# Kernel optimization log

Hardware: AMD Instinct MI355X
Metric: run time of the kernel (lower is better)

## Reference

```python
import jax, jax.numpy as jnp
import numpy as np

N_HEADS = 16
NEG_BIAS = -1000000000.0


def setup_inputs() -> dict:
    key = jax.random.key(0)
    k1, k2, k3, k4 = jax.random.split(key, 4)
    B, S, D = 2, 2048, 1024
    queries = jax.random.normal(k1, (B, S, D), dtype=jnp.float32)
    keys = jax.random.normal(k2, (B, S, D), dtype=jnp.float32)
    values = jax.random.normal(k3, (B, S, D), dtype=jnp.float32)
    mask = jax.random.randint(k4, (B, S, S), 0, 2, dtype=jnp.int32)
    return {"queries": queries, "keys": keys, "values": values, "mask": mask}


def _split_heads(x):
    B, S, D = x.shape
    return x.reshape(B, S, N_HEADS, D // N_HEADS).transpose(0, 2, 1, 3)  # [B,H,S,d]


def reference(queries, keys, values, mask):
    q = _split_heads(queries)   # [B,H,Sq,d]
    k = _split_heads(keys)      # [B,H,Sk,d]
    v = _split_heads(values)    # [B,H,Sk,d]
    d_head = q.shape[-1]
    # scaled dot product similarity
    sim = jnp.einsum('bhqd,bhkd->bhqk', q, k) / jnp.sqrt(jnp.float32(d_head))
    # additive mask (softmax attention function -> non-hadamard)
    bias = NEG_BIAS * (1.0 - mask.astype(sim.dtype))[:, None]  # [B,1,Sq,Sk]
    sim = sim + bias
    # softmax with max-subtraction (numerically stable, as in original)
    weights = jax.nn.softmax(sim, axis=-1)
    out = jnp.einsum('bhqk,bhkd->bhqd', weights, v)  # [B,H,Sq,d]
    B, H, Sq, d = out.shape
    return out.transpose(0, 2, 1, 3).reshape(B, Sq, H * d)
```

## Files before the change

kernel.cpp:

```cpp
#include <hip/hip_runtime.h>

#define S_LEN 2048
#define D_MODEL 1024
#define DH 64
#define BQ 128
#define BK 128
#define ZSCALE 0.18033688f

using short8 = __attribute__((ext_vector_type(8))) short;
using s4v    = __attribute__((ext_vector_type(4))) short;
using f32x4  = __attribute__((ext_vector_type(4))) float;
using u32x4  = __attribute__((ext_vector_type(4))) unsigned int;

#define BMM(a, b, c) __builtin_amdgcn_mfma_f32_16x16x32_bf16((a), (b), (c), 0, 0, 0)

__device__ __forceinline__ unsigned short f2bf(float x) {
    union { float f; unsigned int u; } c; c.f = x;
    unsigned int u = c.u;
    u += 0x7fffu + ((u >> 16) & 1u);
    return (unsigned short)(u >> 16);
}

__global__ __launch_bounds__(256) void cvt_fused(const float* __restrict__ V,
                                                 const int* __restrict__ M,
                                                 const float* __restrict__ K,
                                                 unsigned short* __restrict__ VT,
                                                 unsigned long long* __restrict__ Mb,
                                                 unsigned short* __restrict__ KB) {
    const int blk = blockIdx.x;
    const int tid = threadIdx.x;
    if (blk < 1024) {
        __shared__ float tsF[64][65];
        const int b  = blk >> 9;
        const int h  = (blk >> 5) & 15;
        const int s0 = (blk & 31) * 64;
        #pragma unroll
        for (int it = 0; it < 2; ++it) {
            int seg = tid + it * 256;
            int s = seg >> 3, d8 = (seg & 7) << 3;
            const float* p = V + (size_t)(b * S_LEN + s0 + s) * D_MODEL + h * DH + d8;
            f32x4 a = *(const f32x4*)p;
            f32x4 c = *(const f32x4*)(p + 4);
            #pragma unroll
            for (int j = 0; j < 4; ++j) { tsF[s][d8 + j] = a[j]; tsF[s][d8 + 4 + j] = c[j]; }
        }
        __syncthreads();
        #pragma unroll
        for (int it = 0; it < 2; ++it) {
            int seg = tid + it * 256;
            int d = seg >> 3, s8 = (seg & 7) << 3;
            short8 w;
            #pragma unroll
            for (int j = 0; j < 8; ++j) w[j] = (short)f2bf(tsF[s8 + j][d]);
            *(short8*)(VT + ((size_t)((b * 16 + h) * 64 + d)) * S_LEN + s0 + s8) = w;
        }
    } else if (blk < 2048) {
        const int pb   = blk - 1024;
        const int wave = tid >> 6, lane = tid & 63;
        const int row  = pb * 4 + wave;
        const int* mp  = M + (size_t)row * S_LEN;
        #pragma unroll 4
        for (int it = 0; it < 32; ++it) {
            int m = mp[it * 64 + lane];
            unsigned long long bal = __ballot(m != 0);
            if (lane == 0) Mb[(size_t)row * 32 + it] = bal;
        }
    } else {
        size_t base = (size_t)(blk - 2048) * 4096;
        #pragma unroll
        for (int it = 0; it < 4; ++it) {
            size_t i = base + ((size_t)(it * 256 + tid)) * 4;
            f32x4 a = *(const f32x4*)(K + i);
            s4v w;
            #pragma unroll
            for (int j = 0; j < 4; ++j) w[j] = (short)f2bf(a[j]);
            *(s4v*)(KB + i) = w;
        }
    }
}

__global__ __launch_bounds__(256) void mha_fwd_v18(
    const float* __restrict__ Q,
    const float* __restrict__ K,
    const unsigned short* __restrict__ KB,
    const unsigned short* __restrict__ VT,
    const unsigned long long* __restrict__ Mb,
    float* __restrict__ O,
    float* __restrict__ PO,
    float* __restrict__ PL,
    int kbf, int split_mode)
{
    __shared__ alignas(16) unsigned short Ks[BK][64];
    __shared__ alignas(16) unsigned short Vt[DH][128];

    const int blk0 = blockIdx.x;
    int blk, b, h, qt, split;
    if (split_mode) {
        blk = ((blk0 & 7) << 7) | (blk0 >> 3);
        b = blk >> 9; h = (blk >> 5) & 15; qt = (blk >> 1) & 15; split = blk & 1;
    } else {
        blk = ((blk0 & 7) << 6) | (blk0 >> 3);
        b = blk >> 8; h = (blk >> 4) & 15; qt = blk & 15; split = 0;
    }
    const int qbase = qt * BQ;
    const int bh  = b * 16 + h;
    const int kb0 = split * (S_LEN / 2);
    const int kbend = split_mode ? kb0 + S_LEN / 2 : S_LEN;

    const int tid  = threadIdx.x;
    const int wave = tid >> 6;
    const int lane = tid & 63;
    const int n16  = lane & 15;
    const int quad = lane >> 4;
    const int bq   = quad << 3;
    const int n7   = n16 & 7;

    const int srow = tid >> 3;
    const int prow = (((srow >> 2) & 1) << 4) | (((srow >> 3) & 3) << 2) | (srow & 3);
    const int vrow = tid >> 4;

    const int kwcol = (((tid & 7) ^ (prow & 7)) << 3);
    const int vwcol = (((tid & 15) ^ vrow) << 3);
    const int krc0  = ((quad ^ n7) << 3);
    const int krc1  = krc0 ^ 32;
    int vrc[4];
    #pragma unroll
    for (int kc = 0; kc < 4; ++kc) vrc[kc] = (((kc * 4 + quad) ^ n16) << 3);

    short8 qf[2][2];
    #pragma unroll
    for (int qg = 0; qg < 2; ++qg) {
        const size_t qoff = (size_t)(b * S_LEN + qbase + wave * 32 + qg * 16 + n16) * D_MODEL
                          + h * DH + quad * 8;
        f32x4 a0 = *(const f32x4*)(Q + qoff);
        f32x4 a1 = *(const f32x4*)(Q + qoff + 4);
        f32x4 a2 = *(const f32x4*)(Q + qoff + 32);
        f32x4 a3 = *(const f32x4*)(Q + qoff + 36);
        short8 q0, q1;
        #pragma unroll
        for (int j = 0; j < 4; ++j) {
            q0[j] = (short)f2bf(a0[j] * ZSCALE); q0[4 + j] = (short)f2bf(a1[j] * ZSCALE);
            q1[j] = (short)f2bf(a2[j] * ZSCALE); q1[4 + j] = (short)f2bf(a3[j] * ZSCALE);
        }
        qf[qg][0] = q0; qf[qg][1] = q1;
    }

    const short8 ones = {0x3F80,0x3F80,0x3F80,0x3F80,0x3F80,0x3F80,0x3F80,0x3F80};

    f32x4 o[2][4], o4[2];
    #pragma unroll
    for (int qg = 0; qg < 2; ++qg) {
        #pragma unroll
        for (int dg = 0; dg < 4; ++dg) o[qg][dg] = f32x4{0.f,0.f,0.f,0.f};
        o4[qg] = f32x4{0.f,0.f,0.f,0.f};
    }

    const unsigned long long* mrow[2];
    #pragma unroll
    for (int qg = 0; qg < 2; ++qg)
        mrow[qg] = Mb + (size_t)(b * S_LEN + qbase + wave * 32 + qg * 16 + n16) * 32;

    const size_t kbase = (size_t)(b * S_LEN) * D_MODEL + h * DH;
    const size_t vbase = (size_t)(bh * 64) * S_LEN;

    short8 ka[4], va[4];
    unsigned long long mw[2][2];
    if (kbf) {
        #pragma unroll
        for (int i = 0; i < 4; ++i)
            ka[i] = *(const short8*)(KB + kbase + (size_t)(kb0 + i * 32 + srow) * D_MODEL + ((tid & 7) << 3));
    } else {
        #pragma unroll
        for (int i = 0; i < 4; ++i) {
            const float* kp = K + kbase + (size_t)(kb0 + i * 32 + srow) * D_MODEL + ((tid & 7) << 3);
            f32x4 p0 = *(const f32x4*)kp, p1 = *(const f32x4*)(kp + 4);
            short8 w;
            #pragma unroll
            for (int j = 0; j < 4; ++j) { w[j] = (short)f2bf(p0[j]); w[4 + j] = (short)f2bf(p1[j]); }
            ka[i] = w;
        }
    }
    #pragma unroll
    for (int i = 0; i < 4; ++i)
        va[i] = *(const short8*)(VT + vbase + (size_t)(vrow + 16 * i) * S_LEN + kb0 + ((tid & 15) << 3));
    {
        const int wi = kb0 >> 6;
        #pragma unroll
        for (int qg = 0; qg < 2; ++qg) { mw[qg][0] = mrow[qg][wi]; mw[qg][1] = mrow[qg][wi + 1]; }
    }

    for (int kb = kb0; kb < kbend; kb += BK) {
        __builtin_amdgcn_s_barrier();
        __builtin_amdgcn_sched_barrier(0);

        #pragma unroll
        for (int i = 0; i < 4; ++i) {
            *(short8*)&Ks[prow + 32 * i][kwcol] = ka[i];
            *(short8*)&Vt[vrow + 16 * i][vwcol] = va[i];
        }

        const int kn = kb + BK;
        const bool more = kn < kbend;
        short8 nka[4], nva[4];
        unsigned long long nmw[2][2];
        if (more) {
            if (kbf) {
                #pragma unroll
                for (int i = 0; i < 4; ++i)
                    nka[i] = *(const short8*)(KB + kbase + (size_t)(kn + i * 32 + srow) * D_MODEL + ((tid & 7) << 3));
            } else {
                #pragma unroll
                for (int i = 0; i < 4; ++i) {
                    const float* kp = K + kbase + (size_t)(kn + i * 32 + srow) * D_MODEL + ((tid & 7) << 3);
                    f32x4 p0 = *(const f32x4*)kp, p1 = *(const f32x4*)(kp + 4);
                    short8 w;
                    #pragma unroll
                    for (int j = 0; j < 4; ++j) { w[j] = (short)f2bf(p0[j]); w[4 + j] = (short)f2bf(p1[j]); }
                    nka[i] = w;
                }
            }
            #pragma unroll
            for (int i = 0; i < 4; ++i)
                nva[i] = *(const short8*)(VT + vbase + (size_t)(vrow + 16 * i) * S_LEN + kn + ((tid & 15) << 3));
            const int wi = kn >> 6;
            #pragma unroll
            for (int qg = 0; qg < 2; ++qg) { nmw[qg][0] = mrow[qg][wi]; nmw[qg][1] = mrow[qg][wi + 1]; }
        }

        unsigned int am[2][4];
        #pragma unroll
        for (int qg = 0; qg < 2; ++qg) {
            am[qg][0] = ((unsigned int)mw[qg][0]) >> bq;
            am[qg][1] = ((unsigned int)(mw[qg][0] >> 32)) >> bq;
            am[qg][2] = ((unsigned int)mw[qg][1]) >> bq;
            am[qg][3] = ((unsigned int)(mw[qg][1] >> 32)) >> bq;
        }

        asm volatile("s_waitcnt lgkmcnt(0)" ::: "memory");
        __builtin_amdgcn_s_barrier();
        __builtin_amdgcn_sched_barrier(0);

        u32x4 Af[2][4];
        auto QKCT = [&](int ct) {
            short8 kf0 = *(const short8*)&Ks[ct * 16 + n16][krc0];
            short8 kf1 = *(const short8*)&Ks[ct * 16 + n16][krc1];
            f32x4 sA = {0.f,0.f,0.f,0.f}, sB = sA;
            sA = BMM(kf0, qf[0][0], sA); sA = BMM(kf1, qf[0][1], sA);
            sB = BMM(kf0, qf[1][0], sB); sB = BMM(kf1, qf[1][1], sB);
            unsigned int puA[4], puB[4];
            #pragma unroll
            for (int r = 0; r < 4; ++r) {
                puA[r] = __float_as_uint(__builtin_amdgcn_exp2f(sA[r]));
                puB[r] = __float_as_uint(__builtin_amdgcn_exp2f(sB[r]));
            }
            const int sel = ct >> 1, sb = (ct & 1) * 4, kc = ct >> 1, ub = (ct & 1) * 2;
            unsigned int nibA = (am[0][sel] >> sb) & 0xFu;
            unsigned int nibB = (am[1][sel] >> sb) & 0xFu;
            unsigned int m8A = ((nibA * 0x00204081u) & 0x01010101u) * 0xFFu;
            unsigned int m8B = ((nibB * 0x00204081u) & 0x01010101u) * 0xFFu;
            Af[0][kc][ub + 0] = __builtin_amdgcn_perm(puA[1], puA[0], 0x07060302u)
                              & __builtin_amdgcn_perm(0u, m8A, 0x01010000u);
            Af[0][kc][ub + 1] = __builtin_amdgcn_perm(puA[3], puA[2], 0x07060302u)
                              & __builtin_amdgcn_perm(0u, m8A, 0x03030202u);
            Af[1][kc][ub + 0] = __builtin_amdgcn_perm(puB[1], puB[0], 0x07060302u)
                              & __builtin_amdgcn_perm(0u, m8B, 0x01010000u);
            Af[1][kc][ub + 1] = __builtin_amdgcn_perm(puB[3], puB[2], 0x07060302u)
                              & __builtin_amdgcn_perm(0u, m8B, 0x03030202u);
        };
        auto PVKC = [&](int kc) {
            short8 v0 = *(const short8*)&Vt[      n16][vrc[kc]];
            short8 v1 = *(const short8*)&Vt[16 + n16][vrc[kc]];
            short8 v2 = *(const short8*)&Vt[32 + n16][vrc[kc]];
            short8 v3 = *(const short8*)&Vt[48 + n16][vrc[kc]];
            union { u32x4 u; short8 s; } c0, c1;
            c0.u = Af[0][kc]; c1.u = Af[1][kc];
            o[0][0] = BMM(c0.s, v0, o[0][0]); o[0][1] = BMM(c0.s, v1, o[0][1]);
            o[0][2] = BMM(c0.s, v2, o[0][2]); o[0][3] = BMM(c0.s, v3, o[0][3]);
            o4[0]   = BMM(c0.s, ones, o4[0]);
            o[1][0] = BMM(c1.s, v0, o[1][0]); o[1][1] = BMM(c1.s, v1, o[1][1]);
            o[1][2] = BMM(c1.s, v2, o[1][2]); o[1][3] = BMM(c1.s, v3, o[1][3]);
            o4[1]   = BMM(c1.s, ones, o4[1]);
        };

        __builtin_amdgcn_s_setprio(1);
        QKCT(0); QKCT(1);
        PVKC(0);
        QKCT(2); QKCT(3);
        PVKC(1);
        QKCT(4); QKCT(5);
        PVKC(2);
        QKCT(6); QKCT(7);
        PVKC(3);
        __builtin_amdgcn_s_setprio(0);

        if (more) {
            #pragma unroll
            for (int i = 0; i < 4; ++i) { ka[i] = nka[i]; va[i] = nva[i]; }
            #pragma unroll
            for (int qg = 0; qg < 2; ++qg) { mw[qg][0] = nmw[qg][0]; mw[qg][1] = nmw[qg][1]; }
        }
    }

    if (PO) {
        const int pblk = (bh * 16 + qt) * 2 + split;
        float* pp = PO + (size_t)pblk * (BQ * DH);
        float* pl = PL + (size_t)pblk * BQ;
        #pragma unroll
        for (int qg = 0; qg < 2; ++qg) {
            #pragma unroll
            for (int r = 0; r < 4; ++r) {
                const int rowin = wave * 32 + qg * 16 + quad * 4 + r;
                float* op = pp + rowin * DH + n16;
                op[0]  = o[qg][0][r];
                op[16] = o[qg][1][r];
                op[32] = o[qg][2][r];
                op[48] = o[qg][3][r];
                if (n16 == 0) pl[rowin] = o4[qg][r];
            }
        }
    } else {
        #pragma unroll
        for (int qg = 0; qg < 2; ++qg) {
            #pragma unroll
            for (int r = 0; r < 4; ++r) {
                float rl = 1.f / o4[qg][r];
                size_t row = (size_t)(b * S_LEN + qbase + wave * 32 + qg * 16 + quad * 4 + r);
                float* op = O + row * D_MODEL + h * DH + n16;
                op[0]  = o[qg][0][r] * rl;
                op[16] = o[qg][1][r] * rl;
                op[32] = o[qg][2][r] * rl;
                op[48] = o[qg][3][r] * rl;
            }
        }
    }
}

__global__ __launch_bounds__(256) void combine_split(
    const float* __restrict__ PO, const float* __restrict__ PL,
    float* __restrict__ O)
{
    const int tq = blockIdx.x;
    const int b = tq >> 8, h = (tq >> 4) & 15, qt = tq & 15;
    const float* p0 = PO + (size_t)tq * 2 * (BQ * DH);
    const float* p1 = p0 + BQ * DH;
    const float* l0 = PL + (size_t)tq * 2 * BQ;
    const float* l1 = l0 + BQ;
    const int t = threadIdx.x;
    #pragma unroll
    for (int k = 0; k < 8; ++k) {
        const int e   = (t + k * 256) * 4;
        const int row = e >> 6, col = e & 63;
        f32x4 a = *(const f32x4*)(p0 + e);
        f32x4 c = *(const f32x4*)(p1 + e);
        const float rl = 1.f / (l0[row] + l1[row]);
        f32x4 r;
        #pragma unroll
        for (int j = 0; j < 4; ++j) r[j] = (a[j] + c[j]) * rl;
        *(f32x4*)(O + (size_t)(b * S_LEN + qt * BQ + row) * D_MODEL + h * DH + col) = r;
    }
}

extern "C" void kernel_launch(void* const* d_in, const int* in_sizes, int n_in,
                              void* d_out, int out_size, void* d_ws, size_t ws_size,
                              hipStream_t stream) {
    const float* Q = (const float*)d_in[0];
    const float* K = (const float*)d_in[1];
    const float* V = (const float*)d_in[2];
    const int*   M = (const int*)d_in[3];
    float*       O = (float*)d_out;

    const size_t NEL = (size_t)2 * S_LEN * D_MODEL;
    const size_t VT_BYTES = NEL * sizeof(unsigned short);
    const size_t KB_BYTES = NEL * sizeof(unsigned short);
    const size_t MB_BYTES = (size_t)2 * S_LEN * 32 * 8;
    const size_t PO_BYTES = (size_t)512 * 2 * BQ * DH * 4;
    const size_t PL_BYTES = (size_t)512 * 2 * BQ * 4;

    if (ws_size >= VT_BYTES + KB_BYTES + MB_BYTES + PO_BYTES + PL_BYTES) {
        unsigned short* VT = (unsigned short*)d_ws;
        unsigned short* KB = (unsigned short*)((char*)d_ws + VT_BYTES);
        unsigned long long* Mb = (unsigned long long*)((char*)d_ws + VT_BYTES + KB_BYTES);
        float* PO = (float*)((char*)d_ws + VT_BYTES + KB_BYTES + MB_BYTES);
        float* PL = (float*)((char*)d_ws + VT_BYTES + KB_BYTES + MB_BYTES + PO_BYTES);
        hipLaunchKernelGGL(cvt_fused, dim3(3072), dim3(256), 0, stream, V, M, K, VT, Mb, KB);
        hipLaunchKernelGGL(mha_fwd_v18, dim3(1024), dim3(256), 0, stream,
                           Q, K, KB, VT, Mb, O, PO, PL, 1, 1);
        hipLaunchKernelGGL(combine_split, dim3(512), dim3(256), 0, stream, PO, PL, O);
    } else if (ws_size >= VT_BYTES + KB_BYTES + MB_BYTES) {
        unsigned short* VT = (unsigned short*)d_ws;
        unsigned short* KB = (unsigned short*)((char*)d_ws + VT_BYTES);
        unsigned long long* Mb = (unsigned long long*)((char*)d_ws + VT_BYTES + KB_BYTES);
        hipLaunchKernelGGL(cvt_fused, dim3(3072), dim3(256), 0, stream, V, M, K, VT, Mb, KB);
        hipLaunchKernelGGL(mha_fwd_v18, dim3(512), dim3(256), 0, stream,
                           Q, K, KB, VT, Mb, O, (float*)0, (float*)0, 1, 0);
    } else {
        unsigned short* VT = (unsigned short*)d_ws;
        unsigned long long* Mb = (unsigned long long*)((char*)d_ws + VT_BYTES);
        hipLaunchKernelGGL(cvt_fused, dim3(2048), dim3(256), 0, stream, V, M, K, VT, Mb, (unsigned short*)0);
        hipLaunchKernelGGL(mha_fwd_v18, dim3(512), dim3(256), 0, stream,
                           Q, K, (const unsigned short*)0, VT, Mb, O, (float*)0, (float*)0, 0, 0);
    }
}
```

Before: 181.4 us.

## Enlarge split-K attention blocks to 512 threads covering 256 query rows

New measurement: 180.7 us. No clear change (-0.4%).

```diff
diff --git a/kernel.cpp b/kernel.cpp
--- a/kernel.cpp
+++ b/kernel.cpp
@@ -3,7 +3,6 @@
 #define S_LEN 2048
 #define D_MODEL 1024
 #define DH 64
-#define BQ 128
 #define BK 128
 #define ZSCALE 0.18033688f
 
@@ -79,33 +78,28 @@
     }
 }
 
-__global__ __launch_bounds__(256) void mha_fwd_v18(
+__global__ __launch_bounds__(512) void mha_fwd_v19(
     const float* __restrict__ Q,
-    const float* __restrict__ K,
     const unsigned short* __restrict__ KB,
     const unsigned short* __restrict__ VT,
     const unsigned long long* __restrict__ Mb,
-    float* __restrict__ O,
     float* __restrict__ PO,
-    float* __restrict__ PL,
-    int kbf, int split_mode)
+    float* __restrict__ PL)
 {
     __shared__ alignas(16) unsigned short Ks[BK][64];
     __shared__ alignas(16) unsigned short Vt[DH][128];
 
     const int blk0 = blockIdx.x;
-    int blk, b, h, qt, split;
-    if (split_mode) {
-        blk = ((blk0 & 7) << 7) | (blk0 >> 3);
-        b = blk >> 9; h = (blk >> 5) & 15; qt = (blk >> 1) & 15; split = blk & 1;
-    } else {
-        blk = ((blk0 & 7) << 6) | (blk0 >> 3);
-        b = blk >> 8; h = (blk >> 4) & 15; qt = blk & 15; split = 0;
-    }
-    const int qbase = qt * BQ;
-    const int bh  = b * 16 + h;
-    const int kb0 = split * (S_LEN / 2);
-    const int kbend = split_mode ? kb0 + S_LEN / 2 : S_LEN;
+    const int blk  = ((blk0 & 7) << 6) | (blk0 >> 3);
+
+    const int b     = blk >> 8;
+    const int h     = (blk >> 4) & 15;
+    const int qt    = (blk >> 1) & 7;
+    const int split = blk & 1;
+    const int qbase = qt * 256;
+    const int bh    = b * 16 + h;
+    const int kb0   = split * (S_LEN / 2);
+    const int kbend = kb0 + S_LEN / 2;
 
     const int tid  = threadIdx.x;
     const int wave = tid >> 6;
@@ -116,11 +110,12 @@
     const int n7   = n16 & 7;
 
     const int srow = tid >> 3;
-    const int prow = (((srow >> 2) & 1) << 4) | (((srow >> 3) & 3) << 2) | (srow & 3);
+    const int prow = ((srow >> 5) << 5) | (((srow >> 2) & 1) << 4)
+                   | (((srow >> 3) & 3) << 2) | (srow & 3);
     const int vrow = tid >> 4;
 
     const int kwcol = (((tid & 7) ^ (prow & 7)) << 3);
-    const int vwcol = (((tid & 15) ^ vrow) << 3);
+    const int vwcol = (((tid & 15) ^ (vrow & 15)) << 3);
     const int krc0  = ((quad ^ n7) << 3);
     const int krc1  = krc0 ^ 32;
     int vrc[4];
@@ -163,26 +158,14 @@
     const size_t kbase = (size_t)(b * S_LEN) * D_MODEL + h * DH;
     const size_t vbase = (size_t)(bh * 64) * S_LEN;
 
-    short8 ka[4], va[4];
+    short8 ka[2], va[2];
     unsigned long long mw[2][2];
-    if (kbf) {
-        #pragma unroll
-        for (int i = 0; i < 4; ++i)
-            ka[i] = *(const short8*)(KB + kbase + (size_t)(kb0 + i * 32 + srow) * D_MODEL + ((tid & 7) << 3));
-    } else {
-        #pragma unroll
-        for (int i = 0; i < 4; ++i) {
-            const float* kp = K + kbase + (size_t)(kb0 + i * 32 + srow) * D_MODEL + ((tid & 7) << 3);
-            f32x4 p0 = *(const f32x4*)kp, p1 = *(const f32x4*)(kp + 4);
-            short8 w;
-            #pragma unroll
-            for (int j = 0; j < 4; ++j) { w[j] = (short)f2bf(p0[j]); w[4 + j] = (short)f2bf(p1[j]); }
-            ka[i] = w;
-        }
-    }
-    #pragma unroll
-    for (int i = 0; i < 4; ++i)
-        va[i] = *(const short8*)(VT + vbase + (size_t)(vrow + 16 * i) * S_LEN + kb0 + ((tid & 15) << 3));
+    #pragma unroll
+    for (int i = 0; i < 2; ++i)
+        ka[i] = *(const short8*)(KB + kbase + (size_t)(kb0 + i * 64 + srow) * D_MODEL + ((tid & 7) << 3));
+    #pragma unroll
+    for (int i = 0; i < 2; ++i)
+        va[i] = *(const short8*)(VT + vbase + (size_t)(vrow + 32 * i) * S_LEN + kb0 + ((tid & 15) << 3));
     {
         const int wi = kb0 >> 6;
         #pragma unroll
@@ -194,34 +177,22 @@
         __builtin_amdgcn_sched_barrier(0);
 
         #pragma unroll
-        for (int i = 0; i < 4; ++i) {
-            *(short8*)&Ks[prow + 32 * i][kwcol] = ka[i];
-            *(short8*)&Vt[vrow + 16 * i][vwcol] = va[i];
+        for (int i = 0; i < 2; ++i) {
+            *(short8*)&Ks[prow + 64 * i][kwcol] = ka[i];
+            *(short8*)&Vt[vrow + 32 * i][vwcol] = va[i];
         }
 
         const int kn = kb + BK;
         const bool more = kn < kbend;
-        short8 nka[4], nva[4];
+        short8 nka[2], nva[2];
         unsigned long long nmw[2][2];
         if (more) {
-            if (kbf) {
-                #pragma unroll
-                for (int i = 0; i < 4; ++i)
-                    nka[i] = *(const short8*)(KB + kbase + (size_t)(kn + i * 32 + srow) * D_MODEL + ((tid & 7) << 3));
-            } else {
-                #pragma unroll
-                for (int i = 0; i < 4; ++i) {
-                    const float* kp = K + kbase + (size_t)(kn + i * 32 + srow) * D_MODEL + ((tid & 7) << 3);
-                    f32x4 p0 = *(const f32x4*)kp, p1 = *(const f32x4*)(kp + 4);
-                    short8 w;
-                    #pragma unroll
-                    for (int j = 0; j < 4; ++j) { w[j] = (short)f2bf(p0[j]); w[4 + j] = (short)f2bf(p1[j]); }
-                    nka[i] = w;
-                }
-            }
-            #pragma unroll
-            for (int i = 0; i < 4; ++i)
-                nva[i] = *(const short8*)(VT + vbase + (size_t)(vrow + 16 * i) * S_LEN + kn + ((tid & 15) << 3));
+            #pragma unroll
+            for (int i = 0; i < 2; ++i)
+                nka[i] = *(const short8*)(KB + kbase + (size_t)(kn + i * 64 + srow) * D_MODEL + ((tid & 7) << 3));
+            #pragma unroll
+            for (int i = 0; i < 2; ++i)
+                nva[i] = *(const short8*)(VT + vbase + (size_t)(vrow + 32 * i) * S_LEN + kn + ((tid & 15) << 3));
             const int wi = kn >> 6;
             #pragma unroll
             for (int qg = 0; qg < 2; ++qg) { nmw[qg][0] = mrow[qg][wi]; nmw[qg][1] = mrow[qg][wi + 1]; }
@@ -295,16 +266,16 @@
 
         if (more) {
             #pragma unroll
-            for (int i = 0; i < 4; ++i) { ka[i] = nka[i]; va[i] = nva[i]; }
+            for (int i = 0; i < 2; ++i) { ka[i] = nka[i]; va[i] = nva[i]; }
             #pragma unroll
             for (int qg = 0; qg < 2; ++qg) { mw[qg][0] = nmw[qg][0]; mw[qg][1] = nmw[qg][1]; }
         }
     }
 
-    if (PO) {
-        const int pblk = (bh * 16 + qt) * 2 + split;
-        float* pp = PO + (size_t)pblk * (BQ * DH);
-        float* pl = PL + (size_t)pblk * BQ;
+    {
+        const int pblk = ((bh * 8 + qt) << 1) + split;
+        float* pp = PO + (size_t)pblk * (256 * DH);
+        float* pl = PL + (size_t)pblk * 256;
         #pragma unroll
         for (int qg = 0; qg < 2; ++qg) {
             #pragma unroll
@@ -318,36 +289,22 @@
                 if (n16 == 0) pl[rowin] = o4[qg][r];
             }
         }
-    } else {
-        #pragma unroll
-        for (int qg = 0; qg < 2; ++qg) {
-            #pragma unroll
-            for (int r = 0; r < 4; ++r) {
-                float rl = 1.f / o4[qg][r];
-                size_t row = (size_t)(b * S_LEN + qbase + wave * 32 + qg * 16 + quad * 4 + r);
-                float* op = O + row * D_MODEL + h * DH + n16;
-                op[0]  = o[qg][0][r] * rl;
-                op[16] = o[qg][1][r] * rl;
-                op[32] = o[qg][2][r] * rl;
-                op[48] = o[qg][3][r] * rl;
-            }
-        }
     }
 }
 
-__global__ __launch_bounds__(256) void combine_split(
+__global__ __launch_bounds__(256) void combine_split2(
     const float* __restrict__ PO, const float* __restrict__ PL,
     float* __restrict__ O)
 {
     const int tq = blockIdx.x;
-    const int b = tq >> 8, h = (tq >> 4) & 15, qt = tq & 15;
-    const float* p0 = PO + (size_t)tq * 2 * (BQ * DH);
-    const float* p1 = p0 + BQ * DH;
-    const float* l0 = PL + (size_t)tq * 2 * BQ;
-    const float* l1 = l0 + BQ;
+    const int b = tq >> 7, h = (tq >> 3) & 15, qt = tq & 7;
+    const float* p0 = PO + (size_t)tq * 2 * (256 * DH);
+    const float* p1 = p0 + 256 * DH;
+    const float* l0 = PL + (size_t)tq * 2 * 256;
+    const float* l1 = l0 + 256;
     const int t = threadIdx.x;
     #pragma unroll
-    for (int k = 0; k < 8; ++k) {
+    for (int k = 0; k < 16; ++k) {
         const int e   = (t + k * 256) * 4;
         const int row = e >> 6, col = e & 63;
         f32x4 a = *(const f32x4*)(p0 + e);
@@ -356,7 +313,227 @@
         f32x4 r;
         #pragma unroll
         for (int j = 0; j < 4; ++j) r[j] = (a[j] + c[j]) * rl;
-        *(f32x4*)(O + (size_t)(b * S_LEN + qt * BQ + row) * D_MODEL + h * DH + col) = r;
+        *(f32x4*)(O + (size_t)(b * S_LEN + qt * 256 + row) * D_MODEL + h * DH + col) = r;
+    }
+}
+
+__global__ __launch_bounds__(256) void mha_fwd_v15f(
+    const float* __restrict__ Q,
+    const float* __restrict__ K,
+    const unsigned short* __restrict__ KB,
+    const unsigned short* __restrict__ VT,
+    const unsigned long long* __restrict__ Mb,
+    float* __restrict__ O,
+    int kbf)
+{
+    __shared__ alignas(16) unsigned short Ks[BK][64];
+    __shared__ alignas(16) unsigned short Vt[DH][128];
+
+    const int blk0 = blockIdx.x;
+    const int blk  = ((blk0 & 7) << 6) | (blk0 >> 3);
+    const int b   = blk >> 8;
+    const int h   = (blk >> 4) & 15;
+    const int qbase = (blk & 15) * 128;
+    const int bh  = b * 16 + h;
+
+    const int tid  = threadIdx.x;
+    const int wave = tid >> 6;
+    const int lane = tid & 63;
+    const int n16  = lane & 15;
+    const int quad = lane >> 4;
+    const int bq   = quad << 3;
+    const int n7   = n16 & 7;
+
+    const int srow = tid >> 3;
+    const int prow = (((srow >> 2) & 1) << 4) | (((srow >> 3) & 3) << 2) | (srow & 3);
+    const int vrow = tid >> 4;
+    const int kwcol = (((tid & 7) ^ (prow & 7)) << 3);
+    const int vwcol = (((tid & 15) ^ vrow) << 3);
+    const int krc0  = ((quad ^ n7) << 3);
+    const int krc1  = krc0 ^ 32;
+    int vrc[4];
+    #pragma unroll
+    for (int kc = 0; kc < 4; ++kc) vrc[kc] = (((kc * 4 + quad) ^ n16) << 3);
+
+    short8 qf[2][2];
+    #pragma unroll
+    for (int qg = 0; qg < 2; ++qg) {
+        const size_t qoff = (size_t)(b * S_LEN + qbase + wave * 32 + qg * 16 + n16) * D_MODEL
+                          + h * DH + quad * 8;
+        f32x4 a0 = *(const f32x4*)(Q + qoff);
+        f32x4 a1 = *(const f32x4*)(Q + qoff + 4);
+        f32x4 a2 = *(const f32x4*)(Q + qoff + 32);
+        f32x4 a3 = *(const f32x4*)(Q + qoff + 36);
+        short8 q0, q1;
+        #pragma unroll
+        for (int j = 0; j < 4; ++j) {
+            q0[j] = (short)f2bf(a0[j] * ZSCALE); q0[4 + j] = (short)f2bf(a1[j] * ZSCALE);
+            q1[j] = (short)f2bf(a2[j] * ZSCALE); q1[4 + j] = (short)f2bf(a3[j] * ZSCALE);
+        }
+        qf[qg][0] = q0; qf[qg][1] = q1;
+    }
+
+    const short8 ones = {0x3F80,0x3F80,0x3F80,0x3F80,0x3F80,0x3F80,0x3F80,0x3F80};
+
+    f32x4 o[2][4], o4[2];
+    #pragma unroll
+    for (int qg = 0; qg < 2; ++qg) {
+        #pragma unroll
+        for (int dg = 0; dg < 4; ++dg) o[qg][dg] = f32x4{0.f,0.f,0.f,0.f};
+        o4[qg] = f32x4{0.f,0.f,0.f,0.f};
+    }
+
+    const unsigned long long* mrow[2];
+    #pragma unroll
+    for (int qg = 0; qg < 2; ++qg)
+        mrow[qg] = Mb + (size_t)(b * S_LEN + qbase + wave * 32 + qg * 16 + n16) * 32;
+
+    const size_t kbase = (size_t)(b * S_LEN) * D_MODEL + h * DH;
+    const size_t vbase = (size_t)(bh * 64) * S_LEN;
+
+    short8 ka[4], va[4];
+    unsigned long long mw[2][2];
+    if (kbf) {
+        #pragma unroll
+        for (int i = 0; i < 4; ++i)
+            ka[i] = *(const short8*)(KB + kbase + (size_t)(i * 32 + srow) * D_MODEL + ((tid & 7) << 3));
+    } else {
+        #pragma unroll
+        for (int i = 0; i < 4; ++i) {
+            const float* kp = K + kbase + (size_t)(i * 32 + srow) * D_MODEL + ((tid & 7) << 3);
+            f32x4 p0 = *(const f32x4*)kp, p1 = *(const f32x4*)(kp + 4);
+            short8 w;
+            #pragma unroll
+            for (int j = 0; j < 4; ++j) { w[j] = (short)f2bf(p0[j]); w[4 + j] = (short)f2bf(p1[j]); }
+            ka[i] = w;
+        }
+    }
+    #pragma unroll
+    for (int i = 0; i < 4; ++i)
+        va[i] = *(const short8*)(VT + vbase + (size_t)(vrow + 16 * i) * S_LEN + ((tid & 15) << 3));
+    #pragma unroll
+    for (int qg = 0; qg < 2; ++qg) { mw[qg][0] = mrow[qg][0]; mw[qg][1] = mrow[qg][1]; }
+
+    for (int kb = 0; kb < S_LEN; kb += BK) {
+        __builtin_amdgcn_s_barrier();
+        __builtin_amdgcn_sched_barrier(0);
+        #pragma unroll
+        for (int i = 0; i < 4; ++i) {
+            *(short8*)&Ks[prow + 32 * i][kwcol] = ka[i];
+            *(short8*)&Vt[vrow + 16 * i][vwcol] = va[i];
+        }
+        const int kn = kb + BK;
+        const bool more = kn < S_LEN;
+        short8 nka[4], nva[4];
+        unsigned long long nmw[2][2];
+        if (more) {
+            if (kbf) {
+                #pragma unroll
+                for (int i = 0; i < 4; ++i)
+                    nka[i] = *(const short8*)(KB + kbase + (size_t)(kn + i * 32 + srow) * D_MODEL + ((tid & 7) << 3));
+            } else {
+                #pragma unroll
+                for (int i = 0; i < 4; ++i) {
+                    const float* kp = K + kbase + (size_t)(kn + i * 32 + srow) * D_MODEL + ((tid & 7) << 3);
+                    f32x4 p0 = *(const f32x4*)kp, p1 = *(const f32x4*)(kp + 4);
+                    short8 w;
+                    #pragma unroll
+                    for (int j = 0; j < 4; ++j) { w[j] = (short)f2bf(p0[j]); w[4 + j] = (short)f2bf(p1[j]); }
+                    nka[i] = w;
+                }
+            }
+            #pragma unroll
+            for (int i = 0; i < 4; ++i)
+                nva[i] = *(const short8*)(VT + vbase + (size_t)(vrow + 16 * i) * S_LEN + kn + ((tid & 15) << 3));
+            const int wi = kn >> 6;
+            #pragma unroll
+            for (int qg = 0; qg < 2; ++qg) { nmw[qg][0] = mrow[qg][wi]; nmw[qg][1] = mrow[qg][wi + 1]; }
+        }
+        unsigned int am[2][4];
+        #pragma unroll
+        for (int qg = 0; qg < 2; ++qg) {
+            am[qg][0] = ((unsigned int)mw[qg][0]) >> bq;
+            am[qg][1] = ((unsigned int)(mw[qg][0] >> 32)) >> bq;
+            am[qg][2] = ((unsigned int)mw[qg][1]) >> bq;
+            am[qg][3] = ((unsigned int)(mw[qg][1] >> 32)) >> bq;
+        }
+        asm volatile("s_waitcnt lgkmcnt(0)" ::: "memory");
+        __builtin_amdgcn_s_barrier();
+        __builtin_amdgcn_sched_barrier(0);
+
+        u32x4 Af[2][4];
+        auto QKCT = [&](int ct) {
+            short8 kf0 = *(const short8*)&Ks[ct * 16 + n16][krc0];
+            short8 kf1 = *(const short8*)&Ks[ct * 16 + n16][krc1];
+            f32x4 sA = {0.f,0.f,0.f,0.f}, sB = sA;
+            sA = BMM(kf0, qf[0][0], sA); sA = BMM(kf1, qf[0][1], sA);
+            sB = BMM(kf0, qf[1][0], sB); sB = BMM(kf1, qf[1][1], sB);
+            unsigned int puA[4], puB[4];
+            #pragma unroll
+            for (int r = 0; r < 4; ++r) {
+                puA[r] = __float_as_uint(__builtin_amdgcn_exp2f(sA[r]));
+                puB[r] = __float_as_uint(__builtin_amdgcn_exp2f(sB[r]));
+            }
+            const int sel = ct >> 1, sb = (ct & 1) * 4, kc = ct >> 1, ub = (ct & 1) * 2;
+            unsigned int nibA = (am[0][sel] >> sb) & 0xFu;
+            unsigned int nibB = (am[1][sel] >> sb) & 0xFu;
+            unsigned int m8A = ((nibA * 0x00204081u) & 0x01010101u) * 0xFFu;
+            unsigned int m8B = ((nibB * 0x00204081u) & 0x01010101u) * 0xFFu;
+            Af[0][kc][ub + 0] = __builtin_amdgcn_perm(puA[1], puA[0], 0x07060302u)
+                              & __builtin_amdgcn_perm(0u, m8A, 0x01010000u);
+            Af[0][kc][ub + 1] = __builtin_amdgcn_perm(puA[3], puA[2], 0x07060302u)
+                              & __builtin_amdgcn_perm(0u, m8A, 0x03030202u);
+            Af[1][kc][ub + 0] = __builtin_amdgcn_perm(puB[1], puB[0], 0x07060302u)
+                              & __builtin_amdgcn_perm(0u, m8B, 0x01010000u);
+            Af[1][kc][ub + 1] = __builtin_amdgcn_perm(puB[3], puB[2], 0x07060302u)
+                              & __builtin_amdgcn_perm(0u, m8B, 0x03030202u);
+        };
+        auto PVKC = [&](int kc) {
+            short8 v0 = *(const short8*)&Vt[      n16][vrc[kc]];
+            short8 v1 = *(const short8*)&Vt[16 + n16][vrc[kc]];
+            short8 v2 = *(const short8*)&Vt[32 + n16][vrc[kc]];
+            short8 v3 = *(const short8*)&Vt[48 + n16][vrc[kc]];
+            union { u32x4 u; short8 s; } c0, c1;
+            c0.u = Af[0][kc]; c1.u = Af[1][kc];
+            o[0][0] = BMM(c0.s, v0, o[0][0]); o[0][1] = BMM(c0.s, v1, o[0][1]);
+            o[0][2] = BMM(c0.s, v2, o[0][2]); o[0][3] = BMM(c0.s, v3, o[0][3]);
+            o4[0]   = BMM(c0.s, ones, o4[0]);
+            o[1][0] = BMM(c1.s, v0, o[1][0]); o[1][1] = BMM(c1.s, v1, o[1][1]);
+            o[1][2] = BMM(c1.s, v2, o[1][2]); o[1][3] = BMM(c1.s, v3, o[1][3]);
+            o4[1]   = BMM(c1.s, ones, o4[1]);
+        };
+
+        __builtin_amdgcn_s_setprio(1);
+        QKCT(0); QKCT(1);
+        PVKC(0);
+        QKCT(2); QKCT(3);
+        PVKC(1);
+        QKCT(4); QKCT(5);
+        PVKC(2);
+        QKCT(6); QKCT(7);
+        PVKC(3);
+        __builtin_amdgcn_s_setprio(0);
+
+        if (more) {
+            #pragma unroll
+            for (int i = 0; i < 4; ++i) { ka[i] = nka[i]; va[i] = nva[i]; }
+            #pragma unroll
+            for (int qg = 0; qg < 2; ++qg) { mw[qg][0] = nmw[qg][0]; mw[qg][1] = nmw[qg][1]; }
+        }
+    }
+
+    #pragma unroll
+    for (int qg = 0; qg < 2; ++qg) {
+        #pragma unroll
+        for (int r = 0; r < 4; ++r) {
+            float rl = 1.f / o4[qg][r];
+            size_t row = (size_t)(b * S_LEN + qbase + wave * 32 + qg * 16 + quad * 4 + r);
+            float* op = O + row * D_MODEL + h * DH + n16;
+            op[0]  = o[qg][0][r] * rl;
+            op[16] = o[qg][1][r] * rl;
+            op[32] = o[qg][2][r] * rl;
+            op[48] = o[qg][3][r] * rl;
+        }
     }
 }
 
@@ -373,8 +550,8 @@
     const size_t VT_BYTES = NEL * sizeof(unsigned short);
     const size_t KB_BYTES = NEL * sizeof(unsigned short);
     const size_t MB_BYTES = (size_t)2 * S_LEN * 32 * 8;
-    const size_t PO_BYTES = (size_t)512 * 2 * BQ * DH * 4;
-    const size_t PL_BYTES = (size_t)512 * 2 * BQ * 4;
+    const size_t PO_BYTES = (size_t)512 * 256 * DH * 4;
+    const size_t PL_BYTES = (size_t)512 * 256 * 4;
 
     if (ws_size >= VT_BYTES + KB_BYTES + MB_BYTES + PO_BYTES + PL_BYTES) {
         unsigned short* VT = (unsigned short*)d_ws;
@@ -383,21 +560,21 @@
         float* PO = (float*)((char*)d_ws + VT_BYTES + KB_BYTES + MB_BYTES);
         float* PL = (float*)((char*)d_ws + VT_BYTES + KB_BYTES + MB_BYTES + PO_BYTES);
         hipLaunchKernelGGL(cvt_fused, dim3(3072), dim3(256), 0, stream, V, M, K, VT, Mb, KB);
-        hipLaunchKernelGGL(mha_fwd_v18, dim3(1024), dim3(256), 0, stream,
-                           Q, K, KB, VT, Mb, O, PO, PL, 1, 1);
-        hipLaunchKernelGGL(combine_split, dim3(512), dim3(256), 0, stream, PO, PL, O);
+        hipLaunchKernelGGL(mha_fwd_v19, dim3(512), dim3(512), 0, stream,
+                           Q, KB, VT, Mb, PO, PL);
+        hipLaunchKernelGGL(combine_split2, dim3(256), dim3(256), 0, stream, PO, PL, O);
     } else if (ws_size >= VT_BYTES + KB_BYTES + MB_BYTES) {
         unsigned short* VT = (unsigned short*)d_ws;
         unsigned short* KB = (unsigned short*)((char*)d_ws + VT_BYTES);
         unsigned long long* Mb = (unsigned long long*)((char*)d_ws + VT_BYTES + KB_BYTES);
         hipLaunchKernelGGL(cvt_fused, dim3(3072), dim3(256), 0, stream, V, M, K, VT, Mb, KB);
-        hipLaunchKernelGGL(mha_fwd_v18, dim3(512), dim3(256), 0, stream,
-                           Q, K, KB, VT, Mb, O, (float*)0, (float*)0, 1, 0);
+        hipLaunchKernelGGL(mha_fwd_v15f, dim3(512), dim3(256), 0, stream,
+                           Q, K, KB, VT, Mb, O, 1);
     } else {
         unsigned short* VT = (unsigned short*)d_ws;
         unsigned long long* Mb = (unsigned long long*)((char*)d_ws + VT_BYTES);
         hipLaunchKernelGGL(cvt_fused, dim3(2048), dim3(256), 0, stream, V, M, K, VT, Mb, (unsigned short*)0);
-        hipLaunchKernelGGL(mha_fwd_v18, dim3(512), dim3(256), 0, stream,
-                           Q, K, (const unsigned short*)0, VT, Mb, O, (float*)0, (float*)0, 0, 0);
+        hipLaunchKernelGGL(mha_fwd_v15f, dim3(512), dim3(256), 0, stream,
+                           Q, K, (unsigned short*)0, VT, Mb, O, 0);
     }
 }
```
